# Kernel tuning notes

Measured on AMD Instinct MI355X. Metric: run time of the kernel, lower is better.

## Reference

```python
import jax, jax.numpy as jnp
import numpy as np

N = 50000      # nodes
E = 640000     # edges
FIN = 100      # raw node feature dim (nn.Linear(100, d_model))
D = 128        # d_model (dim_hidden)
H = 8          # num_heads
DH = D // H    # head dim
L = 4          # num_layers
DFF = 4 * D    # dim_feedforward
G = 64         # number of graphs in the batch
SCALE = DH ** -0.5


def setup_inputs() -> dict:
    key = jax.random.key(0)
    ks = jax.random.split(key, 12)
    x = jax.random.normal(ks[0], (N, FIN), jnp.float32)
    edge_index = jax.random.randint(ks[1], (2, E), 0, N, dtype=jnp.int64)
    batch = jnp.sort(jax.random.randint(ks[2], (N,), 0, G, dtype=jnp.int64))

    def w(k, shape, fan_in):
        return jax.random.normal(k, shape, jnp.float32) * (fan_in ** -0.5)

    W_embed = w(ks[3], (FIN, D), FIN)          # embedding, bias=False
    Wqk = w(ks[4], (L, D, 2 * D), D)           # to_qk, bias=False
    Wv = w(ks[5], (L, D, D), D)                # to_v, bias=False
    Wout = w(ks[6], (L, D, D), D)              # out_proj
    b_out = jnp.zeros((L, D), jnp.float32)
    W1 = w(ks[7], (L, D, DFF), D)              # FFN linear1
    b1 = jnp.zeros((L, DFF), jnp.float32)
    W2 = w(ks[8], (L, DFF, D), DFF)            # FFN linear2
    b2 = jnp.zeros((L, D), jnp.float32)
    return dict(x=x, edge_index=edge_index, batch=batch, W_embed=W_embed,
                Wqk=Wqk, Wv=Wv, Wout=Wout, b_out=b_out, W1=W1, b1=b1,
                W2=W2, b2=b2)


def reference(x, edge_index, batch, W_embed, Wqk, Wv, Wout, b_out, W1, b1, W2, b2):
    src = edge_index[0]  # j (message source)
    dst = edge_index[1]  # i (aggregation target)
    h = x @ W_embed  # [N, D]; dropout is identity at eval
    for l in range(L):
        # --- DAG multi-head attention (PyG MessagePassing, aggr='add') ---
        qk = h @ Wqk[l]
        q, k = qk[:, :D], qk[:, D:]
        v = h @ Wv[l]
        qj = q[src].reshape(E, H, DH)   # qk_j: gathered at source
        ki = k[dst].reshape(E, H, DH)   # qk_i: gathered at target
        logits = (qj * ki).sum(-1) * SCALE  # [E, H]
        # segment softmax over edges sharing the same target node
        m = jax.ops.segment_max(logits, dst, num_segments=N)        # [N, H]
        p = jnp.exp(logits - m[dst])
        ssum = jax.ops.segment_sum(p, dst, num_segments=N)          # [N, H]
        attn = p / ssum[dst]
        msg = (v[src].reshape(E, H, DH) * attn[:, :, None]).reshape(E, D)
        agg = jax.ops.segment_sum(msg, dst, num_segments=N)         # [N, D]
        h = h + (agg @ Wout[l] + b_out[l])   # residual; norm1 = Identity
        # --- FFN (relu) ---
        ff = jax.nn.relu(h @ W1[l] + b1[l]) @ W2[l] + b2[l]
        h = h + ff                            # residual; norm2 = Identity
    # global mean pool over graphs
    cnt = jax.ops.segment_sum(jnp.ones((N,), h.dtype), batch, num_segments=G)
    pooled = jax.ops.segment_sum(h, batch, num_segments=G) / jnp.maximum(cnt, 1.0)[:, None]
    return pooled
```

## Files before the change

### kernel.cpp

```cpp
#include <hip/hip_runtime.h>
#include <hip/hip_bf16.h>
#include <math.h>

#define D 128
#define NH 8
#define DFF 512
#define NG 64
#define NL 4
#define FIN 100
#define SCALE 0.25f
#define QKV 384

typedef __attribute__((ext_vector_type(8))) short short8;
typedef __attribute__((ext_vector_type(4))) float f32x4;

__device__ inline unsigned short f2bf(float v) {
    __hip_bfloat16 b = __float2bfloat16(v);
    return *reinterpret_cast<unsigned short*>(&b);
}

__global__ void count_kernel(const int* __restrict__ dst, int* __restrict__ cnt, int E) {
    int e = blockIdx.x * 256 + threadIdx.x;
    if (e < E) atomicAdd(&cnt[dst[e]], 1);
}

__global__ __launch_bounds__(1024) void scan_block_kernel(const int* __restrict__ cnt,
        int* __restrict__ incl, int* __restrict__ partials, int n) {
    __shared__ int s[1024];
    int tid = threadIdx.x;
    int gid = blockIdx.x * 1024 + tid;
    int val = (gid < n) ? cnt[gid] : 0;
    s[tid] = val;
    __syncthreads();
    for (int o = 1; o < 1024; o <<= 1) {
        int t = (tid >= o) ? s[tid - o] : 0;
        __syncthreads();
        s[tid] += t;
        __syncthreads();
    }
    if (gid < n) incl[gid] = s[tid];
    if (tid == 1023) partials[blockIdx.x] = s[1023];
}

__global__ void scan_partials_kernel(int* __restrict__ partials, int nb) {
    if (threadIdx.x == 0 && blockIdx.x == 0) {
        int run = 0;
        for (int i = 0; i < nb; ++i) { int t = partials[i]; partials[i] = run; run += t; }
    }
}

__global__ void finalize_off_kernel(const int* __restrict__ cnt, const int* __restrict__ incl,
        const int* __restrict__ partials, int* __restrict__ off, int* __restrict__ cur,
        int n, int E) {
    int gid = blockIdx.x * 256 + threadIdx.x;
    if (gid < n) {
        int v = incl[gid] - cnt[gid] + partials[gid >> 10];
        off[gid] = v;
        cur[gid] = v;
    }
    if (gid == 0) off[n] = E;
}

__global__ void scatter_kernel(const int* __restrict__ src, const int* __restrict__ dst,
        int* __restrict__ cur, int* __restrict__ csr_src, int E) {
    int e = blockIdx.x * 256 + threadIdx.x;
    if (e < E) {
        int p = atomicAdd(&cur[dst[e]], 1);
        csr_src[p] = src[e];
    }
}

__global__ void transpose_cvt_kernel(const float* __restrict__ W, __hip_bfloat16* __restrict__ Bt,
        int K, int N, int ldl) {
    int l = blockIdx.y;
    const float* w = W + (size_t)l * K * N;
    __hip_bfloat16* bt = Bt + (size_t)l * ldl;
    int idx = blockIdx.x * 256 + threadIdx.x;
    if (idx >= K * N) return;
    int n = idx / K, k = idx - n * K;
    bt[(size_t)n * K + k] = __float2bfloat16(w[(size_t)k * N + n]);
}

__global__ void pad_cvt_x_kernel(const float* __restrict__ x, __hip_bfloat16* __restrict__ xb, int n) {
    int idx = blockIdx.x * 256 + threadIdx.x;
    if (idx >= n * 128) return;
    int r = idx >> 7, c = idx & 127;
    xb[idx] = (c < FIN) ? __float2bfloat16(x[(size_t)r * FIN + c]) : __float2bfloat16(0.f);
}

__global__ void wembT_kernel(const float* __restrict__ W, __hip_bfloat16* __restrict__ Bt) {
    int idx = blockIdx.x * 256 + threadIdx.x;
    if (idx >= 128 * 128) return;
    int n = idx >> 7, k = idx & 127;
    Bt[idx] = (k < FIN) ? __float2bfloat16(W[(size_t)k * 128 + n]) : __float2bfloat16(0.f);
}

__global__ __launch_bounds__(256) void gemm_mfma(
        const __hip_bfloat16* __restrict__ A, const __hip_bfloat16* __restrict__ Bt,
        float* __restrict__ Cf, __hip_bfloat16* __restrict__ Cb,
        int M, int N, int K) {
    __shared__ __align__(16) unsigned short As[128][64];
    __shared__ __align__(16) unsigned short Bs[64][64];
    int t = threadIdx.x;
    int wave = t >> 6, lane = t & 63;
    int row0 = blockIdx.x * 128, col0 = blockIdx.y * 64;
    f32x4 acc[2][4] = {};

    int sr = t >> 3;
    int sc = t & 7;

    for (int k0 = 0; k0 < K; k0 += 64) {
#pragma unroll
        for (int i = 0; i < 4; ++i) {
            int r = i * 32 + sr;
            int gr = row0 + r;
            if (gr >= M) gr = M - 1;
            *reinterpret_cast<short8*>(&As[r][(sc ^ (r & 7)) << 3]) =
                *reinterpret_cast<const short8*>(&A[(size_t)gr * K + k0 + (sc << 3)]);
        }
#pragma unroll
        for (int i = 0; i < 2; ++i) {
            int r = i * 32 + sr;
            *reinterpret_cast<short8*>(&Bs[r][(sc ^ (r & 7)) << 3]) =
                *reinterpret_cast<const short8*>(&Bt[(size_t)(col0 + r) * K + k0 + (sc << 3)]);
        }
        __syncthreads();
#pragma unroll
        for (int kk = 0; kk < 64; kk += 32) {
            int lr = lane & 15;
            int kc = (kk >> 3) + (lane >> 4);
            short8 a[2], b[4];
#pragma unroll
            for (int m = 0; m < 2; ++m) {
                int r = wave * 32 + m * 16 + lr;
                a[m] = *reinterpret_cast<const short8*>(&As[r][(kc ^ (r & 7)) << 3]);
            }
#pragma unroll
            for (int n = 0; n < 4; ++n) {
                int r = n * 16 + lr;
                b[n] = *reinterpret_cast<const short8*>(&Bs[r][(kc ^ (r & 7)) << 3]);
            }
#pragma unroll
            for (int m = 0; m < 2; ++m)
#pragma unroll
                for (int n = 0; n < 4; ++n)
                    acc[m][n] = __builtin_amdgcn_mfma_f32_16x16x32_bf16(a[m], b[n], acc[m][n], 0, 0, 0);
        }
        __syncthreads();
    }

    int lr = lane & 15, rg = (lane >> 4) * 4;
#pragma unroll
    for (int m = 0; m < 2; ++m) {
#pragma unroll
        for (int n = 0; n < 4; ++n) {
            int col = col0 + n * 16 + lr;
#pragma unroll
            for (int j = 0; j < 4; ++j) {
                int row = row0 + wave * 32 + m * 16 + rg + j;
                if (row < M) {
                    float val = acc[m][n][j];
                    Cf[(size_t)row * N + col] = val;
                    Cb[(size_t)row * N + col] = __float2bfloat16(val);
                }
            }
        }
    }
}

__global__ __launch_bounds__(256, 3) void gemm_qkv(
        const __hip_bfloat16* __restrict__ A, const __hip_bfloat16* __restrict__ Bt,
        __hip_bfloat16* __restrict__ Cb, int M) {
    __shared__ __align__(16) unsigned short As[128 * 128];
    __shared__ __align__(16) unsigned short Bs[64 * 128];
    int t = threadIdx.x;
    int wave = t >> 6, lane = t & 63;
    int lr = lane & 15, lg = lane >> 4;
    int row0 = blockIdx.x * 128;

#pragma unroll
    for (int i = 0; i < 8; ++i) {
        int idx = t + i * 256;
        int r = idx >> 4, ch = idx & 15;
        int gr = row0 + r; if (gr >= M) gr = M - 1;
        *reinterpret_cast<short8*>(&As[r * 128 + ((ch ^ (r & 7)) << 3)]) =
            *reinterpret_cast<const short8*>(&A[(size_t)gr * 128 + ch * 8]);
    }

    short8 a_all[2][4];
    for (int c = 0; c < 6; ++c) {
#pragma unroll
        for (int i = 0; i < 4; ++i) {
            int idx = t + i * 256;
            int r = idx >> 4, ch = idx & 15;
            *reinterpret_cast<short8*>(&Bs[r * 128 + ((ch ^ (r & 7)) << 3)]) =
                *reinterpret_cast<const short8*>(&Bt[((size_t)(c * 64 + r)) * 128 + ch * 8]);
        }
        __syncthreads();
        if (c == 0) {
#pragma unroll
            for (int m = 0; m < 2; ++m)
#pragma unroll
                for (int ks = 0; ks < 4; ++ks) {
                    int r = wave * 32 + m * 16 + lr;
                    int kc = ks * 4 + lg;
                    a_all[m][ks] = *reinterpret_cast<const short8*>(&As[r * 128 + ((kc ^ (r & 7)) << 3)]);
                }
        }
        f32x4 acc[2][4] = {};
#pragma unroll
        for (int ks = 0; ks < 4; ++ks) {
            int kc = ks * 4 + lg;
            short8 b[4];
#pragma unroll
            for (int n = 0; n < 4; ++n) {
                int r = n * 16 + lr;
                b[n] = *reinterpret_cast<const short8*>(&Bs[r * 128 + ((kc ^ (r & 7)) << 3)]);
            }
#pragma unroll
            for (int m = 0; m < 2; ++m)
#pragma unroll
                for (int n = 0; n < 4; ++n)
                    acc[m][n] = __builtin_amdgcn_mfma_f32_16x16x32_bf16(a_all[m][ks], b[n], acc[m][n], 0, 0, 0);
        }
#pragma unroll
        for (int m = 0; m < 2; ++m)
#pragma unroll
            for (int n = 0; n < 4; ++n) {
                int col = c * 64 + n * 16 + lr;
#pragma unroll
                for (int j = 0; j < 4; ++j) {
                    int row = row0 + wave * 32 + m * 16 + lg * 4 + j;
                    if (row < M)
                        Cb[(size_t)row * QKV + col] = __float2bfloat16(acc[m][n][j]);
                }
            }
        __syncthreads();
    }
}

__global__ __launch_bounds__(256) void fused_out_ffn(
        const __hip_bfloat16* __restrict__ aggb, const __hip_bfloat16* __restrict__ WoutT,
        const float* __restrict__ b_out,
        const __hip_bfloat16* __restrict__ W1T, const float* __restrict__ b1,
        const __hip_bfloat16* __restrict__ W2T, const float* __restrict__ b2,
        float* __restrict__ h32, __hip_bfloat16* __restrict__ hb, int M) {
    extern __shared__ __align__(16) unsigned short smem[];
    unsigned short* As  = smem;
    unsigned short* Bs  = smem + 16384;
    unsigned short* W1s = Bs;
    unsigned short* ff1s = Bs + 8192;
    unsigned short* W2s = smem + 32768;

    int t = threadIdx.x;
    int wave = t >> 6, lane = t & 63;
    int lr = lane & 15, lg = lane >> 4;
    int row0 = blockIdx.x * 128;

#pragma unroll
    for (int i = 0; i < 8; ++i) {
        int idx = t + i * 256;
        int r = idx >> 4, ch = idx & 15;
        int gr = row0 + r; if (gr >= M) gr = M - 1;
        *reinterpret_cast<short8*>(&As[r * 128 + ((ch ^ (r & 7)) << 3)]) =
            *reinterpret_cast<const short8*>(&aggb[(size_t)gr * 128 + ch * 8]);
        *reinterpret_cast<short8*>(&Bs[r * 128 + ((ch ^ (r & 7)) << 3)]) =
            *reinterpret_cast<const short8*>(&WoutT[(size_t)r * 128 + ch * 8]);
    }
    __syncthreads();

    f32x4 acc1[2][8] = {};
#pragma unroll
    for (int kk4 = 0; kk4 < 4; ++kk4) {
        int kc = kk4 * 4 + lg;
        short8 a[2], b[8];
#pragma unroll
        for (int m = 0; m < 2; ++m) {
            int r = wave * 32 + m * 16 + lr;
            a[m] = *reinterpret_cast<const short8*>(&As[r * 128 + ((kc ^ (r & 7)) << 3)]);
        }
#pragma unroll
        for (int n = 0; n < 8; ++n) {
            int r = n * 16 + lr;
            b[n] = *reinterpret_cast<const short8*>(&Bs[r * 128 + ((kc ^ (r & 7)) << 3)]);
        }
#pragma unroll
        for (int m = 0; m < 2; ++m)
#pragma unroll
            for (int n = 0; n < 8; ++n)
                acc1[m][n] = __builtin_amdgcn_mfma_f32_16x16x32_bf16(a[m], b[n], acc1[m][n], 0, 0, 0);
    }

#pragma unroll
    for (int m = 0; m < 2; ++m) {
#pragma unroll
        for (int n = 0; n < 8; ++n) {
            int col = n * 16 + lr;
            float bo = b_out[col];
#pragma unroll
            for (int j = 0; j < 4; ++j) {
                int rl = wave * 32 + m * 16 + lg * 4 + j;
                int row = row0 + rl;
                float hv = (row < M) ? h32[(size_t)row * 128 + col] : 0.f;
                float val = acc1[m][n][j] + bo + hv;
                acc1[m][n][j] = val;
                As[rl * 128 + (((col >> 3) ^ (rl & 7)) << 3) + (col & 7)] = f2bf(val);
            }
        }
    }

    short8 a_ff[2][4];
#pragma unroll
    for (int m = 0; m < 2; ++m)
#pragma unroll
        for (int ks = 0; ks < 4; ++ks) {
            int r = wave * 32 + m * 16 + lr;
            int kc = ks * 4 + lg;
            a_ff[m][ks] = *reinterpret_cast<const short8*>(&As[r * 128 + ((kc ^ (r & 7)) << 3)]);
        }
    __syncthreads();

    for (int c = 0; c < 8; ++c) {
        if (c > 0) __syncthreads();
#pragma unroll
        for (int i = 0; i < 4; ++i) {
            int idx = t + i * 256;
            int r = idx >> 4, ch = idx & 15;
            *reinterpret_cast<short8*>(&W1s[r * 128 + ((ch ^ (r & 7)) << 3)]) =
                *reinterpret_cast<const short8*>(&W1T[((size_t)(c * 64 + r)) * 128 + ch * 8]);
        }
#pragma unroll
        for (int i = 0; i < 4; ++i) {
            int idx = t + i * 256;
            int r = idx >> 3, ch = idx & 7;
            *reinterpret_cast<short8*>(&W2s[r * 64 + ((ch ^ (r & 7)) << 3)]) =
                *reinterpret_cast<const short8*>(&W2T[(size_t)r * 512 + c * 64 + ch * 8]);
        }
        __syncthreads();
        f32x4 acc2[2][4] = {};
#pragma unroll
        for (int kk4 = 0; kk4 < 4; ++kk4) {
            short8 b[4];
#pragma unroll
            for (int n = 0; n < 4; ++n) {
                int r = n * 16 + lr;
                int kc = kk4 * 4 + lg;
                b[n] = *reinterpret_cast<const short8*>(&W1s[r * 128 + ((kc ^ (r & 7)) << 3)]);
            }
#pragma unroll
            for (int m = 0; m < 2; ++m)
#pragma unroll
                for (int n = 0; n < 4; ++n)
                    acc2[m][n] = __builtin_amdgcn_mfma_f32_16x16x32_bf16(a_ff[m][kk4], b[n], acc2[m][n], 0, 0, 0);
        }
#pragma unroll
        for (int m = 0; m < 2; ++m) {
#pragma unroll
            for (int n = 0; n < 4; ++n) {
                int col = n * 16 + lr;
                float bb = b1[c * 64 + col];
#pragma unroll
                for (int j = 0; j < 4; ++j) {
                    int rl = wave * 32 + m * 16 + lg * 4 + j;
                    float val = fmaxf(acc2[m][n][j] + bb, 0.f);
                    ff1s[rl * 64 + (((col >> 3) ^ (rl & 7)) << 3) + (col & 7)] = f2bf(val);
                }
            }
        }
#pragma unroll
        for (int kk4 = 0; kk4 < 2; ++kk4) {
            int kc = kk4 * 4 + lg;
            short8 a[2], b[8];
#pragma unroll
            for (int m = 0; m < 2; ++m) {
                int r = wave * 32 + m * 16 + lr;
                a[m] = *reinterpret_cast<const short8*>(&ff1s[r * 64 + ((kc ^ (r & 7)) << 3)]);
            }
#pragma unroll
            for (int n = 0; n < 8; ++n) {
                int r = n * 16 + lr;
                b[n] = *reinterpret_cast<const short8*>(&W2s[r * 64 + ((kc ^ (r & 7)) << 3)]);
            }
#pragma unroll
            for (int m = 0; m < 2; ++m)
#pragma unroll
                for (int n = 0; n < 8; ++n)
                    acc1[m][n] = __builtin_amdgcn_mfma_f32_16x16x32_bf16(a[m], b[n], acc1[m][n], 0, 0, 0);
        }
    }

#pragma unroll
    for (int m = 0; m < 2; ++m) {
#pragma unroll
        for (int n = 0; n < 8; ++n) {
            int col = n * 16 + lr;
            float bb = b2[col];
#pragma unroll
            for (int j = 0; j < 4; ++j) {
                int row = row0 + wave * 32 + m * 16 + lg * 4 + j;
                if (row < M) {
                    float val = acc1[m][n][j] + bb;
                    h32[(size_t)row * 128 + col] = val;
                    hb[(size_t)row * 128 + col] = __float2bfloat16(val);
                }
            }
        }
    }
}

__global__ __launch_bounds__(256) void attn_kernel(const __hip_bfloat16* __restrict__ qkvb,
        const int* __restrict__ off, const int* __restrict__ csr_src,
        __hip_bfloat16* __restrict__ aggb, int n) {
    int wave = threadIdx.x >> 6;
    int lane = threadIdx.x & 63;
    int i = blockIdx.x * 4 + wave;
    if (i >= n) return;
    const unsigned* qv = reinterpret_cast<const unsigned*>(qkvb);
    unsigned ku = qv[(size_t)i * 192 + 64 + lane];
    float kx = __uint_as_float(ku << 16);
    float ky = __uint_as_float(ku & 0xffff0000u);
    int e0 = off[i], e1 = off[i + 1];
    float m = -INFINITY, ssum = 0.f, ax = 0.f, ay = 0.f;
    int e = e0;
    for (; e + 4 <= e1; e += 4) {
        int s0 = csr_src[e], s1 = csr_src[e + 1], s2 = csr_src[e + 2], s3 = csr_src[e + 3];
        unsigned q0 = qv[(size_t)s0 * 192 + lane];
        unsigned q1 = qv[(size_t)s1 * 192 + lane];
        unsigned q2 = qv[(size_t)s2 * 192 + lane];
        unsigned q3 = qv[(size_t)s3 * 192 + lane];
        unsigned w0 = qv[(size_t)s0 * 192 + 128 + lane];
        unsigned w1 = qv[(size_t)s1 * 192 + 128 + lane];
        unsigned w2 = qv[(size_t)s2 * 192 + 128 + lane];
        unsigned w3 = qv[(size_t)s3 * 192 + 128 + lane];
        float l0 = __uint_as_float(q0 << 16) * kx + __uint_as_float(q0 & 0xffff0000u) * ky;
        float l1 = __uint_as_float(q1 << 16) * kx + __uint_as_float(q1 & 0xffff0000u) * ky;
        float l2 = __uint_as_float(q2 << 16) * kx + __uint_as_float(q2 & 0xffff0000u) * ky;
        float l3 = __uint_as_float(q3 << 16) * kx + __uint_as_float(q3 & 0xffff0000u) * ky;
        l0 += __shfl_xor(l0, 1); l1 += __shfl_xor(l1, 1); l2 += __shfl_xor(l2, 1); l3 += __shfl_xor(l3, 1);
        l0 += __shfl_xor(l0, 2); l1 += __shfl_xor(l1, 2); l2 += __shfl_xor(l2, 2); l3 += __shfl_xor(l3, 2);
        l0 += __shfl_xor(l0, 4); l1 += __shfl_xor(l1, 4); l2 += __shfl_xor(l2, 4); l3 += __shfl_xor(l3, 4);
        l0 *= SCALE; l1 *= SCALE; l2 *= SCALE; l3 *= SCALE;
        float mx = fmaxf(fmaxf(l0, l1), fmaxf(l2, l3));
        float mn = fmaxf(m, mx);
        float corr = __expf(m - mn);
        float p0 = __expf(l0 - mn);
        float p1 = __expf(l1 - mn);
        float p2 = __expf(l2 - mn);
        float p3 = __expf(l3 - mn);
        ssum = ssum * corr + ((p0 + p1) + (p2 + p3));
        ax = ax * corr + p0 * __uint_as_float(w0 << 16) + p1 * __uint_as_float(w1 << 16)
                       + p2 * __uint_as_float(w2 << 16) + p3 * __uint_as_float(w3 << 16);
        ay = ay * corr + p0 * __uint_as_float(w0 & 0xffff0000u) + p1 * __uint_as_float(w1 & 0xffff0000u)
                       + p2 * __uint_as_float(w2 & 0xffff0000u) + p3 * __uint_as_float(w3 & 0xffff0000u);
        m = mn;
    }
    for (; e < e1; ++e) {
        int s0 = csr_src[e];
        unsigned q0 = qv[(size_t)s0 * 192 + lane];
        unsigned w0 = qv[(size_t)s0 * 192 + 128 + lane];
        float l0 = __uint_as_float(q0 << 16) * kx + __uint_as_float(q0 & 0xffff0000u) * ky;
        l0 += __shfl_xor(l0, 1); l0 += __shfl_xor(l0, 2); l0 += __shfl_xor(l0, 4);
        l0 *= SCALE;
        float mn = fmaxf(m, l0);
        float corr = __expf(m - mn);
        float pe = __expf(l0 - mn);
        ssum = ssum * corr + pe;
        ax = ax * corr + pe * __uint_as_float(w0 << 16);
        ay = ay * corr + pe * __uint_as_float(w0 & 0xffff0000u);
        m = mn;
    }
    float inv = (ssum > 0.f) ? 1.f / ssum : 0.f;
    __hip_bfloat162 o;
    o.x = __float2bfloat16(ax * inv);
    o.y = __float2bfloat16(ay * inv);
    *reinterpret_cast<__hip_bfloat162*>(aggb + (size_t)i * 128 + lane * 2) = o;
}

__global__ void group_bounds_kernel(const int* __restrict__ batch, int n, int* __restrict__ gstart) {
    int g = threadIdx.x;
    if (g > NG) return;
    int lo = 0, hi = n;
    while (lo < hi) {
        int mid = (lo + hi) >> 1;
        if (batch[mid] < g) lo = mid + 1; else hi = mid;
    }
    gstart[g] = lo;
}

__global__ __launch_bounds__(256) void pool_stage1(const float* __restrict__ h,
        const int* __restrict__ gstart, float* __restrict__ pws) {
    int g = blockIdx.x, sub = blockIdx.y;
    int s = gstart[g], e = gstart[g + 1];
    int c = threadIdx.x & 127;
    int half = threadIdx.x >> 7;
    float acc = 0.f;
    for (int r = s + sub * 2 + half; r < e; r += 16)
        acc += h[(size_t)r * 128 + c];
    __shared__ float tmp[2][128];
    tmp[half][c] = acc;
    __syncthreads();
    if (half == 0)
        pws[((size_t)g * 8 + sub) * 128 + c] = tmp[0][c] + tmp[1][c];
}

__global__ void pool_stage2(const float* __restrict__ pws, const int* __restrict__ gstart,
        float* __restrict__ out) {
    int g = blockIdx.x, c = threadIdx.x;
    float s = 0.f;
#pragma unroll
    for (int i = 0; i < 8; ++i) s += pws[((size_t)g * 8 + i) * 128 + c];
    float cntf = (float)(gstart[g + 1] - gstart[g]);
    out[(size_t)g * 128 + c] = s / fmaxf(cntf, 1.f);
}

extern "C" void kernel_launch(void* const* d_in, const int* in_sizes, int n_in,
                              void* d_out, int out_size, void* d_ws, size_t ws_size,
                              hipStream_t stream) {
    const float* x = (const float*)d_in[0];
    const int* ei = (const int*)d_in[1];
    const int* batch = (const int*)d_in[2];
    const float* W_embed = (const float*)d_in[3];
    const float* Wqk = (const float*)d_in[4];
    const float* Wv = (const float*)d_in[5];
    const float* Wout = (const float*)d_in[6];
    const float* b_out = (const float*)d_in[7];
    const float* W1 = (const float*)d_in[8];
    const float* b1 = (const float*)d_in[9];
    const float* W2 = (const float*)d_in[10];
    const float* b2 = (const float*)d_in[11];

    int Nn = in_sizes[2];
    int E = in_sizes[1] / 2;

    char* p = (char*)d_ws;
    auto alloc = [&](size_t bytes) {
        char* r = p;
        p += (bytes + 255) & ~(size_t)255;
        return r;
    };
    float* h32 = (float*)alloc((size_t)Nn * D * 4);
    __hip_bfloat16* hb = (__hip_bfloat16*)alloc((size_t)Nn * D * 2);
    __hip_bfloat16* aggb = (__hip_bfloat16*)alloc((size_t)Nn * D * 2);
    __hip_bfloat16* qkvb = (__hip_bfloat16*)alloc((size_t)Nn * QKV * 2);
    __hip_bfloat16* xb = (__hip_bfloat16*)alloc((size_t)Nn * D * 2);
    __hip_bfloat16* WembT = (__hip_bfloat16*)alloc((size_t)D * D * 2);
    __hip_bfloat16* WqkvT = (__hip_bfloat16*)alloc((size_t)NL * QKV * D * 2);
    __hip_bfloat16* WoutT = (__hip_bfloat16*)alloc((size_t)NL * D * D * 2);
    __hip_bfloat16* W1T = (__hip_bfloat16*)alloc((size_t)NL * D * DFF * 2);
    __hip_bfloat16* W2T = (__hip_bfloat16*)alloc((size_t)NL * DFF * D * 2);
    int* csr_src = (int*)alloc((size_t)E * 4);
    int* cnt = (int*)alloc((size_t)Nn * 4);
    int* incl = (int*)alloc((size_t)Nn * 4);
    int* off = (int*)alloc(((size_t)Nn + 1) * 4);
    int* cur = (int*)alloc((size_t)Nn * 4);
    int* partials = (int*)alloc(1024 * 4);
    int* gstart = (int*)alloc((NG + 1) * 4);
    float* pws = (float*)alloc((size_t)NG * 8 * 128 * 4);

    const int* e_src = ei;
    const int* e_dst = ei + E;

    hipMemsetAsync(cnt, 0, (size_t)Nn * 4, stream);
    count_kernel<<<(E + 255) / 256, 256, 0, stream>>>(e_dst, cnt, E);
    int nsb = (Nn + 1023) / 1024;
    scan_block_kernel<<<nsb, 1024, 0, stream>>>(cnt, incl, partials, Nn);
    scan_partials_kernel<<<1, 64, 0, stream>>>(partials, nsb);
    finalize_off_kernel<<<(Nn + 255) / 256, 256, 0, stream>>>(cnt, incl, partials, off, cur, Nn, E);
    scatter_kernel<<<(E + 255) / 256, 256, 0, stream>>>(e_src, e_dst, cur, csr_src, E);

    transpose_cvt_kernel<<<dim3((2 * D * D + 255) / 256, NL), 256, 0, stream>>>(
        Wqk, WqkvT, D, 2 * D, QKV * D);
    transpose_cvt_kernel<<<dim3((D * D + 255) / 256, NL), 256, 0, stream>>>(
        Wv, WqkvT + (size_t)2 * D * D, D, D, QKV * D);
    transpose_cvt_kernel<<<dim3((D * D + 255) / 256, NL), 256, 0, stream>>>(
        Wout, WoutT, D, D, D * D);
    transpose_cvt_kernel<<<dim3((D * DFF + 255) / 256, NL), 256, 0, stream>>>(
        W1, W1T, D, DFF, D * DFF);
    transpose_cvt_kernel<<<dim3((DFF * D + 255) / 256, NL), 256, 0, stream>>>(
        W2, W2T, DFF, D, DFF * D);
    wembT_kernel<<<(128 * 128 + 255) / 256, 256, 0, stream>>>(W_embed, WembT);
    pad_cvt_x_kernel<<<((size_t)Nn * 128 + 255) / 256, 256, 0, stream>>>(x, xb, Nn);

    int gmb = (Nn + 127) / 128;
    gemm_mfma<<<dim3(gmb, D / 64), 256, 0, stream>>>(xb, WembT, h32, hb, Nn, D, D);

    size_t fused_lds = (size_t)(16384 + 16384 + 8192) * sizeof(unsigned short);

    for (int l = 0; l < NL; ++l) {
        gemm_qkv<<<gmb, 256, 0, stream>>>(hb, WqkvT + (size_t)l * QKV * D, qkvb, Nn);
        attn_kernel<<<(Nn + 3) / 4, 256, 0, stream>>>(qkvb, off, csr_src, aggb, Nn);
        fused_out_ffn<<<gmb, 256, fused_lds, stream>>>(
            aggb, WoutT + (size_t)l * D * D, b_out + (size_t)l * D,
            W1T + (size_t)l * D * DFF, b1 + (size_t)l * DFF,
            W2T + (size_t)l * DFF * D, b2 + (size_t)l * D,
            h32, hb, Nn);
    }

    group_bounds_kernel<<<1, 128, 0, stream>>>(batch, Nn, gstart);
    pool_stage1<<<dim3(NG, 8), 256, 0, stream>>>(h32, gstart, pws);
    pool_stage2<<<NG, 128, 0, stream>>>(pws, gstart, (float*)d_out);
}
```

Before: 684.0 us.

## Fuse next-layer QKV projection into out-proj/FFN kernel and shrink LDS footprint

The next layer's QKV GEMM is folded into the tail of the fused out-proj/FFN kernel. The bf16 h stays in LDS as the A operand, which removes three separate gemm_qkv launches and the hb write/read round trip. LDS use drops from 80KB dynamic to 48KB static by loading Wout in two halves and reusing buffers, and launch_bounds(256,3) targets three blocks per CU. The cost is a longer kernel with more syncs and possible register pressure under the tighter occupancy bound.

```diff
diff --git a/kernel.cpp b/kernel.cpp
--- a/kernel.cpp
+++ b/kernel.cpp
@@ -9,7 +9,7 @@
 #define NL 4
 #define FIN 100
 #define SCALE 0.25f
-#define QKV 384
+#define QKVN 384
 
 typedef __attribute__((ext_vector_type(8))) short short8;
 typedef __attribute__((ext_vector_type(4))) float f32x4;
@@ -232,67 +232,72 @@
                 for (int j = 0; j < 4; ++j) {
                     int row = row0 + wave * 32 + m * 16 + lg * 4 + j;
                     if (row < M)
-                        Cb[(size_t)row * QKV + col] = __float2bfloat16(acc[m][n][j]);
+                        Cb[(size_t)row * QKVN + col] = __float2bfloat16(acc[m][n][j]);
                 }
             }
         __syncthreads();
     }
 }
 
-__global__ __launch_bounds__(256) void fused_out_ffn(
+template<bool QKV>
+__global__ __launch_bounds__(256, 3) void fused_out_ffn(
         const __hip_bfloat16* __restrict__ aggb, const __hip_bfloat16* __restrict__ WoutT,
         const float* __restrict__ b_out,
         const __hip_bfloat16* __restrict__ W1T, const float* __restrict__ b1,
         const __hip_bfloat16* __restrict__ W2T, const float* __restrict__ b2,
-        float* __restrict__ h32, __hip_bfloat16* __restrict__ hb, int M) {
-    extern __shared__ __align__(16) unsigned short smem[];
-    unsigned short* As  = smem;
-    unsigned short* Bs  = smem + 16384;
-    unsigned short* W1s = Bs;
-    unsigned short* ff1s = Bs + 8192;
-    unsigned short* W2s = smem + 32768;
+        const __hip_bfloat16* __restrict__ WqkvT, __hip_bfloat16* __restrict__ qkvb,
+        float* __restrict__ h32, int M) {
+    __shared__ __align__(16) unsigned short As[128 * 128];
+    __shared__ __align__(16) unsigned short Bs[64 * 128];
+    unsigned short* ff1s = As;
+    unsigned short* W2s  = As + 8192;
 
     int t = threadIdx.x;
     int wave = t >> 6, lane = t & 63;
     int lr = lane & 15, lg = lane >> 4;
     int row0 = blockIdx.x * 128;
 
-#pragma unroll
-    for (int i = 0; i < 8; ++i) {
-        int idx = t + i * 256;
-        int r = idx >> 4, ch = idx & 15;
-        int gr = row0 + r; if (gr >= M) gr = M - 1;
-        *reinterpret_cast<short8*>(&As[r * 128 + ((ch ^ (r & 7)) << 3)]) =
-            *reinterpret_cast<const short8*>(&aggb[(size_t)gr * 128 + ch * 8]);
-        *reinterpret_cast<short8*>(&Bs[r * 128 + ((ch ^ (r & 7)) << 3)]) =
-            *reinterpret_cast<const short8*>(&WoutT[(size_t)r * 128 + ch * 8]);
-    }
-    __syncthreads();
+    short8 a[2][4];
+#pragma unroll
+    for (int m = 0; m < 2; ++m)
+#pragma unroll
+        for (int ks = 0; ks < 4; ++ks) {
+            int gr = row0 + wave * 32 + m * 16 + lr; if (gr >= M) gr = M - 1;
+            a[m][ks] = *reinterpret_cast<const short8*>(&aggb[(size_t)gr * 128 + (ks * 4 + lg) * 8]);
+        }
 
     f32x4 acc1[2][8] = {};
 #pragma unroll
-    for (int kk4 = 0; kk4 < 4; ++kk4) {
-        int kc = kk4 * 4 + lg;
-        short8 a[2], b[8];
-#pragma unroll
-        for (int m = 0; m < 2; ++m) {
-            int r = wave * 32 + m * 16 + lr;
-            a[m] = *reinterpret_cast<const short8*>(&As[r * 128 + ((kc ^ (r & 7)) << 3)]);
-        }
-#pragma unroll
-        for (int n = 0; n < 8; ++n) {
-            int r = n * 16 + lr;
-            b[n] = *reinterpret_cast<const short8*>(&Bs[r * 128 + ((kc ^ (r & 7)) << 3)]);
-        }
-#pragma unroll
-        for (int m = 0; m < 2; ++m)
-#pragma unroll
-            for (int n = 0; n < 8; ++n)
-                acc1[m][n] = __builtin_amdgcn_mfma_f32_16x16x32_bf16(a[m], b[n], acc1[m][n], 0, 0, 0);
-    }
-
-#pragma unroll
-    for (int m = 0; m < 2; ++m) {
+    for (int half = 0; half < 2; ++half) {
+        if (half == 1) __syncthreads();
+#pragma unroll
+        for (int i = 0; i < 4; ++i) {
+            int idx = t + i * 256;
+            int r = idx >> 4, ch = idx & 15;
+            *reinterpret_cast<short8*>(&Bs[r * 128 + ((ch ^ (r & 7)) << 3)]) =
+                *reinterpret_cast<const short8*>(&WoutT[((size_t)(half * 64 + r)) * 128 + ch * 8]);
+        }
+        __syncthreads();
+#pragma unroll
+        for (int ks = 0; ks < 4; ++ks) {
+            int kc = ks * 4 + lg;
+            short8 b[4];
+#pragma unroll
+            for (int n = 0; n < 4; ++n) {
+                int r = n * 16 + lr;
+                b[n] = *reinterpret_cast<const short8*>(&Bs[r * 128 + ((kc ^ (r & 7)) << 3)]);
+            }
+#pragma unroll
+            for (int m = 0; m < 2; ++m)
+#pragma unroll
+                for (int n = 0; n < 4; ++n)
+                    acc1[m][half * 4 + n] = __builtin_amdgcn_mfma_f32_16x16x32_bf16(
+                        a[m][ks], b[n], acc1[m][half * 4 + n], 0, 0, 0);
+        }
+    }
+
+#pragma unroll
+    for (int m = 0; m < 2; ++m)
 #pragma unroll
         for (int n = 0; n < 8; ++n) {
             int col = n * 16 + lr;
@@ -307,7 +312,6 @@
                 As[rl * 128 + (((col >> 3) ^ (rl & 7)) << 3) + (col & 7)] = f2bf(val);
             }
         }
-    }
 
     short8 a_ff[2][4];
 #pragma unroll
@@ -325,36 +329,32 @@
 #pragma unroll
         for (int i = 0; i < 4; ++i) {
             int idx = t + i * 256;
-            int r = idx >> 4, ch = idx & 15;
-            *reinterpret_cast<short8*>(&W1s[r * 128 + ((ch ^ (r & 7)) << 3)]) =
-                *reinterpret_cast<const short8*>(&W1T[((size_t)(c * 64 + r)) * 128 + ch * 8]);
-        }
-#pragma unroll
-        for (int i = 0; i < 4; ++i) {
-            int idx = t + i * 256;
-            int r = idx >> 3, ch = idx & 7;
-            *reinterpret_cast<short8*>(&W2s[r * 64 + ((ch ^ (r & 7)) << 3)]) =
-                *reinterpret_cast<const short8*>(&W2T[(size_t)r * 512 + c * 64 + ch * 8]);
+            int r1 = idx >> 4, ch1 = idx & 15;
+            *reinterpret_cast<short8*>(&Bs[r1 * 128 + ((ch1 ^ (r1 & 7)) << 3)]) =
+                *reinterpret_cast<const short8*>(&W1T[((size_t)(c * 64 + r1)) * 128 + ch1 * 8]);
+            int r2 = idx >> 3, ch2 = idx & 7;
+            *reinterpret_cast<short8*>(&W2s[r2 * 64 + ((ch2 ^ (r2 & 7)) << 3)]) =
+                *reinterpret_cast<const short8*>(&W2T[(size_t)r2 * 512 + c * 64 + ch2 * 8]);
         }
         __syncthreads();
         f32x4 acc2[2][4] = {};
 #pragma unroll
-        for (int kk4 = 0; kk4 < 4; ++kk4) {
+        for (int ks = 0; ks < 4; ++ks) {
+            int kc = ks * 4 + lg;
             short8 b[4];
 #pragma unroll
             for (int n = 0; n < 4; ++n) {
                 int r = n * 16 + lr;
-                int kc = kk4 * 4 + lg;
-                b[n] = *reinterpret_cast<const short8*>(&W1s[r * 128 + ((kc ^ (r & 7)) << 3)]);
+                b[n] = *reinterpret_cast<const short8*>(&Bs[r * 128 + ((kc ^ (r & 7)) << 3)]);
             }
 #pragma unroll
             for (int m = 0; m < 2; ++m)
 #pragma unroll
                 for (int n = 0; n < 4; ++n)
-                    acc2[m][n] = __builtin_amdgcn_mfma_f32_16x16x32_bf16(a_ff[m][kk4], b[n], acc2[m][n], 0, 0, 0);
-        }
-#pragma unroll
-        for (int m = 0; m < 2; ++m) {
+                    acc2[m][n] = __builtin_amdgcn_mfma_f32_16x16x32_bf16(a_ff[m][ks], b[n], acc2[m][n], 0, 0, 0);
+        }
+#pragma unroll
+        for (int m = 0; m < 2; ++m)
 #pragma unroll
             for (int n = 0; n < 4; ++n) {
                 int col = n * 16 + lr;
@@ -366,44 +366,100 @@
                     ff1s[rl * 64 + (((col >> 3) ^ (rl & 7)) << 3) + (col & 7)] = f2bf(val);
                 }
             }
-        }
-#pragma unroll
-        for (int kk4 = 0; kk4 < 2; ++kk4) {
-            int kc = kk4 * 4 + lg;
-            short8 a[2], b[8];
+#pragma unroll
+        for (int ks = 0; ks < 2; ++ks) {
+            int kc = ks * 4 + lg;
+            short8 a2[2];
 #pragma unroll
             for (int m = 0; m < 2; ++m) {
-                int r = wave * 32 + m * 16 + lr;
-                a[m] = *reinterpret_cast<const short8*>(&ff1s[r * 64 + ((kc ^ (r & 7)) << 3)]);
-            }
-#pragma unroll
-            for (int n = 0; n < 8; ++n) {
-                int r = n * 16 + lr;
-                b[n] = *reinterpret_cast<const short8*>(&W2s[r * 64 + ((kc ^ (r & 7)) << 3)]);
-            }
-#pragma unroll
-            for (int m = 0; m < 2; ++m)
-#pragma unroll
-                for (int n = 0; n < 8; ++n)
-                    acc1[m][n] = __builtin_amdgcn_mfma_f32_16x16x32_bf16(a[m], b[n], acc1[m][n], 0, 0, 0);
-        }
-    }
-
-#pragma unroll
-    for (int m = 0; m < 2; ++m) {
+                int ar = wave * 32 + m * 16 + lr;
+                a2[m] = *reinterpret_cast<const short8*>(&ff1s[ar * 64 + ((kc ^ (ar & 7)) << 3)]);
+            }
+#pragma unroll
+            for (int nh = 0; nh < 2; ++nh) {
+                short8 b[4];
+#pragma unroll
+                for (int n = 0; n < 4; ++n) {
+                    int r = (nh * 4 + n) * 16 + lr;
+                    b[n] = *reinterpret_cast<const short8*>(&W2s[r * 64 + ((kc ^ (r & 7)) << 3)]);
+                }
+#pragma unroll
+                for (int m = 0; m < 2; ++m)
+#pragma unroll
+                    for (int n = 0; n < 4; ++n)
+                        acc1[m][nh * 4 + n] = __builtin_amdgcn_mfma_f32_16x16x32_bf16(
+                            a2[m], b[n], acc1[m][nh * 4 + n], 0, 0, 0);
+            }
+        }
+    }
+    __syncthreads();
+
+#pragma unroll
+    for (int m = 0; m < 2; ++m)
 #pragma unroll
         for (int n = 0; n < 8; ++n) {
             int col = n * 16 + lr;
             float bb = b2[col];
 #pragma unroll
             for (int j = 0; j < 4; ++j) {
-                int row = row0 + wave * 32 + m * 16 + lg * 4 + j;
-                if (row < M) {
-                    float val = acc1[m][n][j] + bb;
-                    h32[(size_t)row * 128 + col] = val;
-                    hb[(size_t)row * 128 + col] = __float2bfloat16(val);
+                int rl = wave * 32 + m * 16 + lg * 4 + j;
+                int row = row0 + rl;
+                float val = acc1[m][n][j] + bb;
+                if (row < M) h32[(size_t)row * 128 + col] = val;
+                if (QKV)
+                    As[rl * 128 + (((col >> 3) ^ (rl & 7)) << 3) + (col & 7)] = f2bf(val);
+            }
+        }
+
+    if (QKV) {
+        short8 a_qv[2][4];
+#pragma unroll
+        for (int m = 0; m < 2; ++m)
+#pragma unroll
+            for (int ks = 0; ks < 4; ++ks) {
+                int r = wave * 32 + m * 16 + lr;
+                int kc = ks * 4 + lg;
+                a_qv[m][ks] = *reinterpret_cast<const short8*>(&As[r * 128 + ((kc ^ (r & 7)) << 3)]);
+            }
+        __syncthreads();
+        for (int c = 0; c < 6; ++c) {
+            if (c > 0) __syncthreads();
+#pragma unroll
+            for (int i = 0; i < 4; ++i) {
+                int idx = t + i * 256;
+                int r = idx >> 4, ch = idx & 15;
+                *reinterpret_cast<short8*>(&Bs[r * 128 + ((ch ^ (r & 7)) << 3)]) =
+                    *reinterpret_cast<const short8*>(&WqkvT[((size_t)(c * 64 + r)) * 128 + ch * 8]);
+            }
+            __syncthreads();
+            f32x4 acc3[2][4] = {};
+#pragma unroll
+            for (int ks = 0; ks < 4; ++ks) {
+                int kc = ks * 4 + lg;
+                short8 b[4];
+#pragma unroll
+                for (int n = 0; n < 4; ++n) {
+                    int r = n * 16 + lr;
+                    b[n] = *reinterpret_cast<const short8*>(&Bs[r * 128 + ((kc ^ (r & 7)) << 3)]);
                 }
-            }
+#pragma unroll
+                for (int m = 0; m < 2; ++m)
+#pragma unroll
+                    for (int n = 0; n < 4; ++n)
+                        acc3[m][n] = __builtin_amdgcn_mfma_f32_16x16x32_bf16(a_qv[m][ks], b[n], acc3[m][n], 0, 0, 0);
+            }
+#pragma unroll
+            for (int m = 0; m < 2; ++m)
+#pragma unroll
+                for (int n = 0; n < 4; ++n) {
+                    int col = c * 64 + n * 16 + lr;
+#pragma unroll
+                    for (int j = 0; j < 4; ++j) {
+                        int row = row0 + wave * 32 + m * 16 + lg * 4 + j;
+                        if (row < M)
+                            qkvb[(size_t)row * QKVN + col] = __float2bfloat16(acc3[m][n][j]);
+                    }
+                }
         }
     }
 }
@@ -541,10 +597,10 @@
     float* h32 = (float*)alloc((size_t)Nn * D * 4);
     __hip_bfloat16* hb = (__hip_bfloat16*)alloc((size_t)Nn * D * 2);
     __hip_bfloat16* aggb = (__hip_bfloat16*)alloc((size_t)Nn * D * 2);
-    __hip_bfloat16* qkvb = (__hip_bfloat16*)alloc((size_t)Nn * QKV * 2);
+    __hip_bfloat16* qkvb = (__hip_bfloat16*)alloc((size_t)Nn * QKVN * 2);
     __hip_bfloat16* xb = (__hip_bfloat16*)alloc((size_t)Nn * D * 2);
     __hip_bfloat16* WembT = (__hip_bfloat16*)alloc((size_t)D * D * 2);
-    __hip_bfloat16* WqkvT = (__hip_bfloat16*)alloc((size_t)NL * QKV * D * 2);
+    __hip_bfloat16* WqkvT = (__hip_bfloat16*)alloc((size_t)NL * QKVN * D * 2);
     __hip_bfloat16* WoutT = (__hip_bfloat16*)alloc((size_t)NL * D * D * 2);
     __hip_bfloat16* W1T = (__hip_bfloat16*)alloc((size_t)NL * D * DFF * 2);
     __hip_bfloat16* W2T = (__hip_bfloat16*)alloc((size_t)NL * DFF * D * 2);
@@ -569,9 +625,9 @@
     scatter_kernel<<<(E + 255) / 256, 256, 0, stream>>>(e_src, e_dst, cur, csr_src, E);
 
     transpose_cvt_kernel<<<dim3((2 * D * D + 255) / 256, NL), 256, 0, stream>>>(
-        Wqk, WqkvT, D, 2 * D, QKV * D);
+        Wqk, WqkvT, D, 2 * D, QKVN * D);
     transpose_cvt_kernel<<<dim3((D * D + 255) / 256, NL), 256, 0, stream>>>(
-        Wv, WqkvT + (size_t)2 * D * D, D, D, QKV * D);
+        Wv, WqkvT + (size_t)2 * D * D, D, D, QKVN * D);
     transpose_cvt_kernel<<<dim3((D * D + 255) / 256, NL), 256, 0, stream>>>(
         Wout, WoutT, D, D, D * D);
     transpose_cvt_kernel<<<dim3((D * DFF + 255) / 256, NL), 256, 0, stream>>>(
@@ -584,16 +640,23 @@
     int gmb = (Nn + 127) / 128;
     gemm_mfma<<<dim3(gmb, D / 64), 256, 0, stream>>>(xb, WembT, h32, hb, Nn, D, D);
 
-    size_t fused_lds = (size_t)(16384 + 16384 + 8192) * sizeof(unsigned short);
+    gemm_qkv<<<gmb, 256, 0, stream>>>(hb, WqkvT, qkvb, Nn);
 
     for (int l = 0; l < NL; ++l) {
-        gemm_qkv<<<gmb, 256, 0, stream>>>(hb, WqkvT + (size_t)l * QKV * D, qkvb, Nn);
         attn_kernel<<<(Nn + 3) / 4, 256, 0, stream>>>(qkvb, off, csr_src, aggb, Nn);
-        fused_out_ffn<<<gmb, 256, fused_lds, stream>>>(
-            aggb, WoutT + (size_t)l * D * D, b_out + (size_t)l * D,
-            W1T + (size_t)l * D * DFF, b1 + (size_t)l * DFF,
-            W2T + (size_t)l * DFF * D, b2 + (size_t)l * D,
-            h32, hb, Nn);
+        if (l < NL - 1) {
+            fused_out_ffn<true><<<gmb, 256, 0, stream>>>(
+                aggb, WoutT + (size_t)l * D * D, b_out + (size_t)l * D,
+                W1T + (size_t)l * D * DFF, b1 + (size_t)l * DFF,
+                W2T + (size_t)l * DFF * D, b2 + (size_t)l * D,
+                WqkvT + (size_t)(l + 1) * QKVN * D, qkvb, h32, Nn);
+        } else {
+            fused_out_ffn<false><<<gmb, 256, 0, stream>>>(
+                aggb, WoutT + (size_t)l * D * D, b_out + (size_t)l * D,
+                W1T + (size_t)l * D * DFF, b1 + (size_t)l * DFF,
+                W2T + (size_t)l * DFF * D, b2 + (size_t)l * D,
+                nullptr, nullptr, h32, Nn);
+        }
     }
 
     group_bounds_kernel<<<1, 128, 0, stream>>>(batch, Nn, gstart);
```

New measurement: 833.4 us. 1.22x slower.
